# Kernel optimization log

Measured on AMD Instinct MI355X. Metric: run time of the kernel, lower is better.

Reference implementation:

```python
import jax, jax.numpy as jnp
import numpy as np

N = 1024      # num_nodes
U = 64        # num_units
IN_DIM = 2    # input feature dim per node
B = 32        # batch
F = IN_DIM + U  # 66, input_size inside _gconv


def _xavier(k, shape):
    fan_in, fan_out = shape[-2], shape[-1]
    std = (2.0 / (fan_in + fan_out)) ** 0.5
    return jax.random.normal(k, shape, jnp.float32) * std


def setup_inputs() -> dict:
    key = jax.random.key(0)
    ks = jax.random.split(key, 14)
    return {
        "inputs": jax.random.normal(ks[0], (B, N * IN_DIM), jnp.float32),
        "hx": jax.random.normal(ks[1], (B, N * U), jnp.float32),
        "adj": jax.random.uniform(ks[2], (2, N, N), jnp.float32),
        "mask": jax.random.uniform(ks[3], (8, N, N), jnp.float32),
        # gate gconv params (output_size = 2U). Note: torch LayerParams caches by
        # shape, so weights_s/weights_i/weights_bp are ONE shared weight, ditto atts/atti.
        "W_ru": _xavier(ks[4], (F, 2 * U)),
        "Watt_ru": _xavier(ks[5], (N, 2 * U, 2 * U)),
        "Watt1_ru": _xavier(ks[6], (N, 2 * U, 1)),
        "Wout_ru": _xavier(ks[7], (6 * U, 2 * U)),
        "b_ru": jnp.ones((2 * U,), jnp.float32),   # bias_start=1.0
        # candidate gconv params (output_size = U)
        "W_c": _xavier(ks[8], (F, U)),
        "Watt_c": _xavier(ks[9], (N, U, U)),
        "Watt1_c": _xavier(ks[10], (N, U, 1)),
        "Wout_c": _xavier(ks[11], (3 * U, U)),
        "b_c": jnp.zeros((U,), jnp.float32),
    }


def _gconv(inputs, state, adj, mask, W, Watt, Watt1, Wout, b):
    Bs = inputs.shape[0]
    x = jnp.concatenate([inputs.reshape(Bs, N, -1), state.reshape(Bs, N, -1)], axis=2)  # [B,N,F]
    Ff = x.shape[2]
    x0 = x.transpose(1, 2, 0).reshape(N, Ff * Bs)  # [N, F*B]
    a0, a1 = adj[0], adj[1]
    # supports in the exact order of the torch loop:
    # adj0, mask0..3*adj0, mask4..7*adj1, adj1  -> 10 matrices
    mats = jnp.concatenate(
        [a0[None], mask[:4] * a0[None], mask[4:] * a1[None], a1[None]], axis=0
    )  # [10,N,N]
    xk = jnp.einsum('mij,jf->mif', mats, x0)  # [10,N,F*B]
    x_all = jnp.concatenate([x0[None], xk], axis=0).reshape(11, N, Ff, Bs)
    x_bp = x_all[0].transpose(2, 0, 1)        # [B,N,F]
    x_i = x_all[1:6].transpose(3, 1, 0, 2)    # [B,N,5,F]
    x_s = x_all[6:].transpose(3, 1, 0, 2)     # [B,N,5,F]
    x_i_p = x_i @ W        # [B,N,5,O] (shared weight, see LayerParams shape cache)
    x_s_p = x_s @ W        # [B,N,5,O]
    x_bp_p = x_bp @ W      # [B,N,O]

    def attend(xp):
        h = jax.nn.relu(jnp.einsum('bnko,noq->bnkq', xp, Watt))     # per-node weights
        s = jnp.einsum('bnkq,nqo->bnko', h, Watt1)[..., 0]          # [B,N,5]
        a = jax.nn.softmax(s, axis=-1)                              # over 5 supports
        return jnp.einsum('bnk,bnko->bno', a, xp)                   # [B,N,O]

    xi = attend(x_i_p)
    xs = attend(x_s_p)
    out = jnp.concatenate([xi, xs, x_bp_p], axis=-1) @ Wout + b     # [B,N,O]
    return out.reshape(Bs, -1)


def reference(inputs, hx, adj, mask, W_ru, Watt_ru, Watt1_ru, Wout_ru, b_ru,
              W_c, Watt_c, Watt1_c, Wout_c, b_c):
    value = jax.nn.sigmoid(_gconv(inputs, hx, adj, mask, W_ru, Watt_ru, Watt1_ru, Wout_ru, b_ru))
    value = value.reshape(-1, N, 2 * U)
    r = value[..., :U].reshape(-1, N * U)
    u = value[..., U:].reshape(-1, N * U)
    c = jnp.tanh(_gconv(inputs, r * hx, adj, mask, W_c, Watt_c, Watt1_c, Wout_c, b_c))
    return u * hx + (1.0 - u) * c
```

## Files before the change

kernel.cpp:

```cpp
#include <hip/hip_runtime.h>
#include <hip/hip_fp16.h>
#include <cstdint>
#include <cstddef>

#define NN 1024
#define BB 32

typedef _Float16 f16x8 __attribute__((ext_vector_type(8)));
typedef _Float16 f16x4 __attribute__((ext_vector_type(4)));
typedef float f32x4 __attribute__((ext_vector_type(4)));

__device__ __forceinline__ void load_lds16(const void* g, void* l) {
  __builtin_amdgcn_global_load_lds(
      (const __attribute__((address_space(1))) void*)g,
      (__attribute__((address_space(3))) void*)l, 16, 0, 0);
}

__global__ __launch_bounds__(256) void k_build_amats(
    const float* __restrict__ adj, const float* __restrict__ mask,
    _Float16* __restrict__ A) {
  int q = blockIdx.x * 256 + threadIdx.x;
  int i = q >> 8;
  int j0 = (q & 255) << 2;
  size_t off = (size_t)i * 1024 + j0;
  float4 a0 = *(const float4*)(adj + off);
  float4 a1 = *(const float4*)(adj + (1u << 20) + off);
  f16x4 r;
  r[0] = a0.x; r[1] = a0.y; r[2] = a0.z; r[3] = a0.w;
  *(f16x4*)(A + off) = r;
  r[0] = a1.x; r[1] = a1.y; r[2] = a1.z; r[3] = a1.w;
  *(f16x4*)(A + (size_t)9 * 1048576 + off) = r;
#pragma unroll
  for (int l = 0; l < 8; ++l) {
    float4 mk = *(const float4*)(mask + (size_t)l * 1048576 + off);
    float4 base = (l < 4) ? a0 : a1;
    r[0] = mk.x * base.x; r[1] = mk.y * base.y;
    r[2] = mk.z * base.z; r[3] = mk.w * base.w;
    *(f16x4*)(A + (size_t)(l + 1) * 1048576 + off) = r;
  }
}

__global__ __launch_bounds__(256) void k_prep_wout(
    const float* __restrict__ Wru, const float* __restrict__ Wc,
    _Float16* __restrict__ WThru, _Float16* __restrict__ WTlru,
    _Float16* __restrict__ WThc, _Float16* __restrict__ WTlc) {
  int id = blockIdx.x * 256 + threadIdx.x;
  if (id < 128 * 384) {
    int o = id & 127, k = id >> 7;
    float w = Wru[k * 128 + o];
    _Float16 h = (_Float16)w;
    WThru[o * 384 + k] = h;
    WTlru[o * 384 + k] = (_Float16)(w - (float)h);
  } else {
    int id2 = id - 128 * 384;
    if (id2 < 64 * 192) {
      int o = id2 & 63, k = id2 >> 6;
      float w = Wc[k * 64 + o];
      _Float16 h = (_Float16)w;
      WThc[o * 192 + k] = h;
      WTlc[o * 192 + k] = (_Float16)(w - (float)h);
    }
  }
}

__global__ __launch_bounds__(256) void k_build_x0p(
    const float* __restrict__ inp, const float* __restrict__ state,
    _Float16* __restrict__ X0P) {
  const int b = blockIdx.x;
  const int j0 = blockIdx.y * 64;
  const int tid = threadIdx.x;
  for (int p = tid; p < 4096; p += 256) {
    int jj = p >> 6, f = p & 63;
    X0P[((size_t)(b * 1024 + j0 + jj)) * 96 + 2 + f] =
        (_Float16)state[(size_t)b * 65536 + (j0 + jj) * 64 + f];
  }
  if (tid < 128) {
    int jj = tid >> 1, f = tid & 1;
    X0P[((size_t)(b * 1024 + j0 + jj)) * 96 + f] =
        (_Float16)inp[(size_t)b * 2048 + (j0 + jj) * 2 + f];
    X0P[((size_t)(b * 1024 + j0 + 32 + jj)) * 96 + f] =
        (_Float16)inp[(size_t)b * 2048 + (j0 + 32 + jj) * 2 + f];
  }
  for (int p = tid; p < 64 * 32; p += 256) {
    int jj = p >> 5, f = 66 + (p & 31);
    if (f < 96)
      X0P[((size_t)(b * 1024 + j0 + jj)) * 96 + f] = (_Float16)0.f;
  }
}

template <int O>
__global__ __launch_bounds__(256, 2) void k_proj0_mfma(
    const _Float16* __restrict__ X0P, const float* __restrict__ W,
    _Float16* __restrict__ XP0, _Float16* __restrict__ XP0T) {
  constexpr int WR = O / 64;
  constexpr int WC = 4 / WR;
  constexpr int TN = WC * 64;
  constexpr int NPT = TN / 64;
  __shared__ _Float16 ldsB[2][TN * 32];
  const int tid = threadIdx.x;
  const int c0 = blockIdx.x * TN;
  const int b = c0 >> 10;
  const int l = tid & 63;
  const int w = tid >> 6;
  const int wr = w / WC, wc = w % WC;

  f16x8 af[4][3];
#pragma unroll
  for (int i = 0; i < 4; ++i) {
    int o = wr * 64 + i * 16 + (l & 15);
#pragma unroll
    for (int ks = 0; ks < 3; ++ks) {
#pragma unroll
      for (int e = 0; e < 8; ++e) {
        int f = ks * 32 + (l >> 4) * 8 + e;
        af[i][ks][e] = (f < 66) ? (_Float16)W[f * O + o] : (_Float16)0.f;
      }
    }
  }

  int tt[NPT], rr[NPT], qq[NPT];
#pragma unroll
  for (int u = 0; u < NPT; ++u) {
    tt[u] = u * 256 + tid;
    rr[u] = tt[u] >> 2;
    qq[u] = (tt[u] & 3) ^ (rr[u] & 3);
  }

  const int ps = ((l >> 4) ^ (l & 3)) * 8;
  int offB[4];
#pragma unroll
  for (int j = 0; j < 4; ++j)
    offB[j] = (wc * 64 + j * 16 + (l & 15)) * 32 + ps;

  f32x4 acc[4][4];
#pragma unroll
  for (int i = 0; i < 4; ++i)
#pragma unroll
    for (int j = 0; j < 4; ++j) acc[i][j] = (f32x4){0.f, 0.f, 0.f, 0.f};

#pragma unroll
  for (int u = 0; u < NPT; ++u)
    load_lds16(X0P + (size_t)(c0 + rr[u]) * 96 + qq[u] * 8,
               &ldsB[0][0] + tt[u] * 8);

  int buf = 0;
  for (int kt = 0; kt < 3; ++kt) {
    __syncthreads();
    if (kt + 1 < 3) {
#pragma unroll
      for (int u = 0; u < NPT; ++u)
        load_lds16(X0P + (size_t)(c0 + rr[u]) * 96 + (kt + 1) * 32 + qq[u] * 8,
                   &ldsB[buf ^ 1][0] + tt[u] * 8);
    }
    f16x8 bf[4];
#pragma unroll
    for (int j = 0; j < 4; ++j) bf[j] = *(const f16x8*)(&ldsB[buf][offB[j]]);
#pragma unroll
    for (int i = 0; i < 4; ++i)
#pragma unroll
      for (int j = 0; j < 4; ++j)
        acc[i][j] = __builtin_amdgcn_mfma_f32_16x16x32_f16(af[i][kt], bf[j],
                                                           acc[i][j], 0, 0, 0);
    buf ^= 1;
  }

#pragma unroll
  for (int i = 0; i < 4; ++i) {
    int ob = wr * 64 + i * 16 + (l >> 4) * 4;
#pragma unroll
    for (int j = 0; j < 4; ++j) {
      int jn = (c0 & 1023) + wc * 64 + j * 16 + (l & 15);
      f16x4 hv;
#pragma unroll
      for (int r = 0; r < 4; ++r) {
        hv[r] = (_Float16)acc[i][j][r];
        XP0T[((size_t)b * O + ob + r) * 1024 + jn] = hv[r];
      }
      *(f16x4*)(XP0 + ((size_t)jn * 32 + b) * O + ob) = hv;
    }
  }
}

template <int CN>
__global__ __launch_bounds__(256, 4) void k_supports2_mfma(
    const _Float16* __restrict__ A, const _Float16* __restrict__ BT,
    _Float16* __restrict__ XPD) {
  __shared__ _Float16 ldsA[2][4096];
  __shared__ _Float16 ldsB[2][4096];
  const int tid = threadIdx.x;
  const int bn = blockIdx.x;
  const int bm = blockIdx.y;
  const int l = tid & 63;
  const int w = tid >> 6;
  const int wr = w >> 1, wc = w & 1;

  const int t0 = tid, t1 = 256 + tid;
  const int r0 = t0 >> 2, q0 = (t0 & 3) ^ (r0 & 3);
  const int r1 = t1 >> 2, q1 = (t1 & 3) ^ (r1 & 3);
  const _Float16* gA0 = A + ((size_t)(bm * 128 + r0)) * 1024 + q0 * 8;
  const _Float16* gA1 = A + ((size_t)(bm * 128 + r1)) * 1024 + q1 * 8;
  const _Float16* gB0 = BT + ((size_t)(bn * 128 + r0)) * 1024 + q0 * 8;
  const _Float16* gB1 = BT + ((size_t)(bn * 128 + r1)) * 1024 + q1 * 8;

  const int ps = ((l >> 4) ^ (l & 3)) * 8;
  int offA[4], offB[4];
#pragma unroll
  for (int i = 0; i < 4; ++i) {
    offA[i] = (wr * 64 + i * 16 + (l & 15)) * 32 + ps;
    offB[i] = (wc * 64 + i * 16 + (l & 15)) * 32 + ps;
  }

  f32x4 acc[4][4];
#pragma unroll
  for (int i = 0; i < 4; ++i)
#pragma unroll
    for (int j = 0; j < 4; ++j) acc[i][j] = (f32x4){0.f, 0.f, 0.f, 0.f};

  load_lds16(gA0, &ldsA[0][0] + t0 * 8);
  load_lds16(gA1, &ldsA[0][0] + t1 * 8);
  load_lds16(gB0, &ldsB[0][0] + t0 * 8);
  load_lds16(gB1, &ldsB[0][0] + t1 * 8);

  int buf = 0;
  for (int kt = 0; kt < 32; ++kt) {
    __syncthreads();
    if (kt + 1 < 32) {
      int k0 = (kt + 1) * 32;
      load_lds16(gA0 + k0, &ldsA[buf ^ 1][0] + t0 * 8);
      load_lds16(gA1 + k0, &ldsA[buf ^ 1][0] + t1 * 8);
      load_lds16(gB0 + k0, &ldsB[buf ^ 1][0] + t0 * 8);
      load_lds16(gB1 + k0, &ldsB[buf ^ 1][0] + t1 * 8);
    }
    f16x8 af[4], bf[4];
#pragma unroll
    for (int i = 0; i < 4; ++i)
      af[i] = *(const f16x8*)(&ldsA[buf][offA[i]]);
#pragma unroll
    for (int i = 0; i < 4; ++i)
      bf[i] = *(const f16x8*)(&ldsB[buf][offB[i]]);
#pragma unroll
    for (int i = 0; i < 4; ++i)
#pragma unroll
      for (int j = 0; j < 4; ++j)
        acc[i][j] = __builtin_amdgcn_mfma_f32_16x16x32_f16(af[i], bf[j],
                                                           acc[i][j], 0, 0, 0);
    buf ^= 1;
  }

#pragma unroll
  for (int i = 0; i < 4; ++i) {
    int R = bm * 128 + wr * 64 + i * 16 + (l >> 4) * 4;
#pragma unroll
    for (int j = 0; j < 4; ++j) {
      int col = bn * 128 + wc * 64 + j * 16 + (l & 15);
#pragma unroll
      for (int r = 0; r < 4; ++r)
        XPD[(size_t)(R + r) * CN + col] = (_Float16)acc[i][j][r];
    }
  }
}

template <int O>
__global__ __launch_bounds__(256) void k_attend_mfma(
    const __half* __restrict__ XPD, const float* __restrict__ Watt,
    const float* __restrict__ Watt1, _Float16* __restrict__ CAT2h,
    _Float16* __restrict__ CAT2l) {
  constexpr int MTW = O / 64;
  constexpr int KS = O / 32;
  constexpr int SLOTS = O / 8;
  constexpr int SWZ = SLOTS - 1;
  const int n = blockIdx.x;
  const int tid = threadIdx.x;
  const int l = tid & 63;
  const int w = tid >> 6;

  __shared__ _Float16 xpL[160 * O];
  __shared__ float sPartL[4][160];
  __shared__ float aL[32][5];

  const int qbase = w * (O / 4);
  f16x8 afr[MTW][KS];
#pragma unroll
  for (int mt = 0; mt < MTW; ++mt) {
    const int q = qbase + mt * 16 + (l & 15);
#pragma unroll
    for (int ks = 0; ks < KS; ++ks) {
#pragma unroll
      for (int e = 0; e < 8; ++e) {
        int o = ks * 32 + (l >> 4) * 8 + e;
        afr[mt][ks][e] = (_Float16)Watt[((size_t)n * O + o) * O + q];
      }
    }
  }
  float wt1[MTW][4];
#pragma unroll
  for (int mt = 0; mt < MTW; ++mt)
#pragma unroll
    for (int r = 0; r < 4; ++r)
      wt1[mt][r] = Watt1[(size_t)n * O + qbase + mt * 16 + (l >> 4) * 4 + r];

  for (int g = 0; g < 2; ++g) {
    if (g) __syncthreads();
    {
      const f16x8* xsrc = reinterpret_cast<const f16x8*>(XPD);
      f16x8* xdst = reinterpret_cast<f16x8*>(xpL);
      for (int p = tid; p < 160 * SLOTS; p += 256) {
        int row = p / SLOTS;
        int sc = p - row * SLOTS;
        int phys = sc ^ (row & SWZ);
        int si = row >> 5, b = row & 31;
        size_t gi = ((size_t)(g * 5 + si) * 1024 + n) * (size_t)(4 * O) +
                    b * (O / 8) + sc;
        xdst[row * SLOTS + phys] = xsrc[gi];
      }
    }
    __syncthreads();

    for (int nt = 0; nt < 10; ++nt) {
      f32x4 acc[MTW];
#pragma unroll
      for (int mt = 0; mt < MTW; ++mt) acc[mt] = (f32x4){0.f, 0.f, 0.f, 0.f};
      const int row = nt * 16 + (l & 15);
#pragma unroll
      for (int ks = 0; ks < KS; ++ks) {
        int phys = (ks * 4 + (l >> 4)) ^ (row & SWZ);
        f16x8 bf = *(const f16x8*)(&xpL[row * O + phys * 8]);
#pragma unroll
        for (int mt = 0; mt < MTW; ++mt)
          acc[mt] = __builtin_amdgcn_mfma_f32_16x16x32_f16(afr[mt][ks], bf,
                                                           acc[mt], 0, 0, 0);
      }
      float sp = 0.f;
#pragma unroll
      for (int mt = 0; mt < MTW; ++mt)
#pragma unroll
        for (int r = 0; r < 4; ++r)
          sp += fmaxf(acc[mt][r], 0.f) * wt1[mt][r];
      sp += __shfl_xor(sp, 16);
      sp += __shfl_xor(sp, 32);
      if (l < 16) sPartL[w][nt * 16 + l] = sp;
    }
    __syncthreads();

    if (tid < 32) {
      const int b = tid;
      float sv[5];
#pragma unroll
      for (int k = 0; k < 5; ++k) {
        int row = k * 32 + b;
        sv[k] = sPartL[0][row] + sPartL[1][row] + sPartL[2][row] +
                sPartL[3][row];
      }
      float mx = sv[0];
#pragma unroll
      for (int k = 1; k < 5; ++k) mx = fmaxf(mx, sv[k]);
      float e[5], sum = 0.f;
#pragma unroll
      for (int k = 0; k < 5; ++k) {
        e[k] = expf(sv[k] - mx);
        sum += e[k];
      }
      float inv = 1.f / sum;
#pragma unroll
      for (int k = 0; k < 5; ++k) aL[b][k] = e[k] * inv;
    }
    __syncthreads();

    for (int it = 0; it < SLOTS * 32 / 256; ++it) {
      int idx = it * 256 + tid;
      int b = idx & 31;
      int sc = idx >> 5;
      float o8[8] = {0.f, 0.f, 0.f, 0.f, 0.f, 0.f, 0.f, 0.f};
#pragma unroll
      for (int si = 0; si < 5; ++si) {
        int row = si * 32 + b;
        int phys = sc ^ (row & SWZ);
        f16x8 xv = *(const f16x8*)(&xpL[row * O + phys * 8]);
        float a = aL[b][si];
#pragma unroll
        for (int j = 0; j < 8; ++j) o8[j] += a * (float)xv[j];
      }
      f16x8 hv, lv;
#pragma unroll
      for (int j = 0; j < 8; ++j) {
        hv[j] = (_Float16)o8[j];
        lv[j] = (_Float16)(o8[j] - (float)hv[j]);
      }
      size_t doff = ((size_t)n * 32 + b) * (2 * O) + g * O + sc * 8;
      *reinterpret_cast<f16x8*>(CAT2h + doff) = hv;
      *reinterpret_cast<f16x8*>(CAT2l + doff) = lv;
    }
  }
}

__global__ __launch_bounds__(256, 2) void k_wout_ru_mfma(
    const _Float16* __restrict__ CAT2h, const _Float16* __restrict__ CAT2l,
    const _Float16* __restrict__ XP0, const _Float16* __restrict__ WTh,
    const _Float16* __restrict__ WTl, const float* __restrict__ bias,
    const float* __restrict__ hx, float* __restrict__ RHX,
    float* __restrict__ UBUF) {
  constexpr int KTOT = 384, KC = 8, KT = 12;
  __shared__ _Float16 ldsAh[2][4096];
  __shared__ _Float16 ldsAl[2][4096];
  __shared__ _Float16 ldsBh[2][4096];
  __shared__ _Float16 ldsBl[2][4096];
  const int tid = threadIdx.x;
  const int blk = blockIdx.x;
  const int l = tid & 63;
  const int w = tid >> 6;
  const int wr = w >> 1, wc = w & 1;

  const int t0 = tid, t1 = 256 + tid;
  const int r0 = t0 >> 2, q0 = (t0 & 3) ^ (r0 & 3);
  const int r1 = t1 >> 2, q1 = (t1 & 3) ^ (r1 & 3);
  const size_t R0 = (size_t)blk * 128 + r0, R1 = (size_t)blk * 128 + r1;
  const _Float16* pA0ch = CAT2h + R0 * 256 + q0 * 8;
  const _Float16* pA1ch = CAT2h + R1 * 256 + q1 * 8;
  const _Float16* pA0cl = CAT2l + R0 * 256 + q0 * 8;
  const _Float16* pA1cl = CAT2l + R1 * 256 + q1 * 8;
  const _Float16* pA0x = XP0 + R0 * 128 + q0 * 8;
  const _Float16* pA1x = XP0 + R1 * 128 + q1 * 8;
  const _Float16* pB0h = WTh + (size_t)r0 * KTOT + q0 * 8;
  const _Float16* pB1h = WTh + (size_t)r1 * KTOT + q1 * 8;
  const _Float16* pB0l = WTl + (size_t)r0 * KTOT + q0 * 8;
  const _Float16* pB1l = WTl + (size_t)r1 * KTOT + q1 * 8;

  const int ps = ((l >> 4) ^ (l & 3)) * 8;
  int offA[4], offB[4];
#pragma unroll
  for (int i = 0; i < 4; ++i) {
    offA[i] = (wr * 64 + i * 16 + (l & 15)) * 32 + ps;
    offB[i] = (wc * 64 + i * 16 + (l & 15)) * 32 + ps;
  }

  f32x4 acc[4][4];
#pragma unroll
  for (int i = 0; i < 4; ++i)
#pragma unroll
    for (int j = 0; j < 4; ++j) acc[i][j] = (f32x4){0.f, 0.f, 0.f, 0.f};

  load_lds16(pA0ch, &ldsAh[0][0] + t0 * 8);
  load_lds16(pA1ch, &ldsAh[0][0] + t1 * 8);
  load_lds16(pA0cl, &ldsAl[0][0] + t0 * 8);
  load_lds16(pA1cl, &ldsAl[0][0] + t1 * 8);
  load_lds16(pB0h, &ldsBh[0][0] + t0 * 8);
  load_lds16(pB1h, &ldsBh[0][0] + t1 * 8);
  load_lds16(pB0l, &ldsBl[0][0] + t0 * 8);
  load_lds16(pB1l, &ldsBl[0][0] + t1 * 8);

  int buf = 0;
  for (int kt = 0; kt < KT; ++kt) {
    __syncthreads();
    if (kt + 1 < KT) {
      int k1 = kt + 1;
      const _Float16* a0 =
          (k1 < KC) ? pA0ch + k1 * 32 : pA0x + (k1 - KC) * 32;
      const _Float16* a1 =
          (k1 < KC) ? pA1ch + k1 * 32 : pA1x + (k1 - KC) * 32;
      load_lds16(a0, &ldsAh[buf ^ 1][0] + t0 * 8);
      load_lds16(a1, &ldsAh[buf ^ 1][0] + t1 * 8);
      if (k1 < KC) {
        load_lds16(pA0cl + k1 * 32, &ldsAl[buf ^ 1][0] + t0 * 8);
        load_lds16(pA1cl + k1 * 32, &ldsAl[buf ^ 1][0] + t1 * 8);
      }
      load_lds16(pB0h + k1 * 32, &ldsBh[buf ^ 1][0] + t0 * 8);
      load_lds16(pB1h + k1 * 32, &ldsBh[buf ^ 1][0] + t1 * 8);
      load_lds16(pB0l + k1 * 32, &ldsBl[buf ^ 1][0] + t0 * 8);
      load_lds16(pB1l + k1 * 32, &ldsBl[buf ^ 1][0] + t1 * 8);
    }
    f16x8 ah[4], bh[4], bl[4];
#pragma unroll
    for (int i = 0; i < 4; ++i) ah[i] = *(const f16x8*)(&ldsAh[buf][offA[i]]);
#pragma unroll
    for (int i = 0; i < 4; ++i) bh[i] = *(const f16x8*)(&ldsBh[buf][offB[i]]);
#pragma unroll
    for (int i = 0; i < 4; ++i) bl[i] = *(const f16x8*)(&ldsBl[buf][offB[i]]);
#pragma unroll
    for (int i = 0; i < 4; ++i)
#pragma unroll
      for (int j = 0; j < 4; ++j) {
        acc[i][j] = __builtin_amdgcn_mfma_f32_16x16x32_f16(ah[i], bh[j],
                                                           acc[i][j], 0, 0, 0);
        acc[i][j] = __builtin_amdgcn_mfma_f32_16x16x32_f16(ah[i], bl[j],
                                                           acc[i][j], 0, 0, 0);
      }
    if (kt < KC) {
      f16x8 al[4];
#pragma unroll
      for (int i = 0; i < 4; ++i)
        al[i] = *(const f16x8*)(&ldsAl[buf][offA[i]]);
#pragma unroll
      for (int i = 0; i < 4; ++i)
#pragma unroll
        for (int j = 0; j < 4; ++j)
          acc[i][j] = __builtin_amdgcn_mfma_f32_16x16x32_f16(al[i], bh[j],
                                                             acc[i][j], 0, 0, 0);
    }
    buf ^= 1;
  }

#pragma unroll
  for (int i = 0; i < 4; ++i) {
    int R = blk * 128 + wr * 64 + i * 16 + (l >> 4) * 4;
#pragma unroll
    for (int j = 0; j < 4; ++j) {
      int o = wc * 64 + j * 16 + (l & 15);
      float bv = bias[o];
#pragma unroll
      for (int rr = 0; rr < 4; ++rr) {
        int Rr = R + rr;
        int n = Rr >> 5, b = Rr & 31;
        size_t base = ((size_t)b * NN + n) * 64;
        float val = 1.f / (1.f + expf(-(acc[i][j][rr] + bv)));
        if (o < 64)
          RHX[base + o] = val * hx[base + o];
        else
          UBUF[base + (o - 64)] = val;
      }
    }
  }
}

__global__ __launch_bounds__(256, 2) void k_wout_c_mfma(
    const _Float16* __restrict__ CAT2h, const _Float16* __restrict__ XP0,
    const _Float16* __restrict__ WTh, const float* __restrict__ bias,
    const float* __restrict__ UBUF, const float* __restrict__ hx,
    float* __restrict__ out) {
  constexpr int KTOT = 192, KC = 4, KT = 6;
  __shared__ _Float16 ldsAh[2][4096];
  __shared__ _Float16 ldsBh[2][2048];
  const int tid = threadIdx.x;
  const int blk = blockIdx.x;
  const int l = tid & 63;
  const int w = tid >> 6;

  const int t0 = tid, t1 = 256 + tid;
  const int r0 = t0 >> 2, q0 = (t0 & 3) ^ (r0 & 3);
  const int r1 = t1 >> 2, q1 = (t1 & 3) ^ (r1 & 3);
  const size_t R0 = (size_t)blk * 128 + r0, R1 = (size_t)blk * 128 + r1;
  const _Float16* pA0ch = CAT2h + R0 * 128 + q0 * 8;
  const _Float16* pA1ch = CAT2h + R1 * 128 + q1 * 8;
  const _Float16* pA0x = XP0 + R0 * 64 + q0 * 8;
  const _Float16* pA1x = XP0 + R1 * 64 + q1 * 8;
  const int rb = tid >> 2, qb = (tid & 3) ^ (rb & 3);
  const _Float16* pBh = WTh + (size_t)rb * KTOT + qb * 8;

  const int ps = ((l >> 4) ^ (l & 3)) * 8;
  int offA[2], offB[4];
#pragma unroll
  for (int i = 0; i < 2; ++i)
    offA[i] = (w * 32 + i * 16 + (l & 15)) * 32 + ps;
#pragma unroll
  for (int j = 0; j < 4; ++j) offB[j] = (j * 16 + (l & 15)) * 32 + ps;

  f32x4 acc[2][4];
#pragma unroll
  for (int i = 0; i < 2; ++i)
#pragma unroll
    for (int j = 0; j < 4; ++j) acc[i][j] = (f32x4){0.f, 0.f, 0.f, 0.f};

  load_lds16(pA0ch, &ldsAh[0][0] + t0 * 8);
  load_lds16(pA1ch, &ldsAh[0][0] + t1 * 8);
  load_lds16(pBh, &ldsBh[0][0] + tid * 8);

  int buf = 0;
  for (int kt = 0; kt < KT; ++kt) {
    __syncthreads();
    if (kt + 1 < KT) {
      int k1 = kt + 1;
      const _Float16* a0 =
          (k1 < KC) ? pA0ch + k1 * 32 : pA0x + (k1 - KC) * 32;
      const _Float16* a1 =
          (k1 < KC) ? pA1ch + k1 * 32 : pA1x + (k1 - KC) * 32;
      load_lds16(a0, &ldsAh[buf ^ 1][0] + t0 * 8);
      load_lds16(a1, &ldsAh[buf ^ 1][0] + t1 * 8);
      load_lds16(pBh + k1 * 32, &ldsBh[buf ^ 1][0] + tid * 8);
    }
    f16x8 ah[2], bh[4];
#pragma unroll
    for (int i = 0; i < 2; ++i) ah[i] = *(const f16x8*)(&ldsAh[buf][offA[i]]);
#pragma unroll
    for (int j = 0; j < 4; ++j) bh[j] = *(const f16x8*)(&ldsBh[buf][offB[j]]);
#pragma unroll
    for (int i = 0; i < 2; ++i)
#pragma unroll
      for (int j = 0; j < 4; ++j)
        acc[i][j] = __builtin_amdgcn_mfma_f32_16x16x32_f16(ah[i], bh[j],
                                                           acc[i][j], 0, 0, 0);
    buf ^= 1;
  }

#pragma unroll
  for (int i = 0; i < 2; ++i) {
    int R = blk * 128 + w * 32 + i * 16 + (l >> 4) * 4;
#pragma unroll
    for (int j = 0; j < 4; ++j) {
      int o = j * 16 + (l & 15);
      float bv = bias[o];
#pragma unroll
      for (int rr = 0; rr < 4; ++rr) {
        int Rr = R + rr;
        int n = Rr >> 5, b = Rr & 31;
        size_t idx = ((size_t)b * NN + n) * 64 + o;
        float cval = tanhf(acc[i][j][rr] + bv);
        float u = UBUF[idx];
        out[idx] = u * hx[idx] + (1.f - u) * cval;
      }
    }
  }
}

extern "C" void kernel_launch(void* const* d_in, const int* in_sizes, int n_in,
                              void* d_out, int out_size, void* d_ws,
                              size_t ws_size, hipStream_t stream) {
  const float* inputs   = (const float*)d_in[0];
  const float* hx       = (const float*)d_in[1];
  const float* adj      = (const float*)d_in[2];
  const float* mask     = (const float*)d_in[3];
  const float* W_ru     = (const float*)d_in[4];
  const float* Watt_ru  = (const float*)d_in[5];
  const float* Watt1_ru = (const float*)d_in[6];
  const float* Wout_ru  = (const float*)d_in[7];
  const float* b_ru     = (const float*)d_in[8];
  const float* W_c      = (const float*)d_in[9];
  const float* Watt_c   = (const float*)d_in[10];
  const float* Watt1_c  = (const float*)d_in[11];
  const float* Wout_c   = (const float*)d_in[12];
  const float* b_c      = (const float*)d_in[13];

  char* ws = (char*)d_ws;
  _Float16*  X0P   = (_Float16*)(ws);
  _Float16*  XPD   = (_Float16*)(ws + 6291456);
  _Float16*  XP0   = (_Float16*)(ws + 90177536);
  _Float16*  XP0T  = (_Float16*)(ws + 98566144);
  _Float16*  CAT2h = (_Float16*)(ws + 106954752);
  _Float16*  CAT2l = (_Float16*)(ws + 123731968);
  float*     RHX   = (float*)(ws + 140509184);
  float*     UBUF  = (float*)(ws + 148897792);
  _Float16*  A_all = (_Float16*)(ws + 157286400);
  _Float16*  WThru = (_Float16*)(ws + 178257920);
  _Float16*  WTlru = (_Float16*)(ws + 178356224);
  _Float16*  WThc  = (_Float16*)(ws + 178454528);
  _Float16*  WTlc  = (_Float16*)(ws + 178479104);
  float*     out   = (float*)d_out;

  k_build_amats<<<1024, 256, 0, stream>>>(adj, mask, A_all);
  k_prep_wout<<<240, 256, 0, stream>>>(Wout_ru, Wout_c, WThru, WTlru, WThc,
                                       WTlc);

  k_build_x0p<<<dim3(32, 16), 256, 0, stream>>>(inputs, hx, X0P);
  k_proj0_mfma<128><<<256, 256, 0, stream>>>(X0P, W_ru, XP0, XP0T);
  k_supports2_mfma<4096><<<dim3(32, 80), 256, 0, stream>>>(A_all, XP0T, XPD);
  k_attend_mfma<128><<<1024, 256, 0, stream>>>((const __half*)XPD, Watt_ru,
                                               Watt1_ru, CAT2h, CAT2l);
  k_wout_ru_mfma<<<256, 256, 0, stream>>>(CAT2h, CAT2l, XP0, WThru, WTlru,
                                          b_ru, hx, RHX, UBUF);
  k_build_x0p<<<dim3(32, 16), 256, 0, stream>>>(inputs, RHX, X0P);
  k_proj0_mfma<64><<<128, 256, 0, stream>>>(X0P, W_c, XP0, XP0T);
  k_supports2_mfma<2048><<<dim3(16, 80), 256, 0, stream>>>(A_all, XP0T, XPD);
  k_attend_mfma<64><<<1024, 256, 0, stream>>>((const __half*)XPD, Watt_c,
                                              Watt1_c, CAT2h, CAT2l);
  k_wout_c_mfma<<<256, 256, 0, stream>>>(CAT2h, XP0, WThc, b_c,
                                         UBUF, hx, out);
}
```

Measured before the change: 340.0 us.

## Fuse x0 packing into projection, merge prep kernels, stage GEMM epilogue via LDS

Merges the adjacency/mask build and the Wout transpose into one prep launch. Folds the fp32-to-fp16 packing of inputs and state directly into the projection kernel, so the X0P buffer and its two build launches go away. The supports GEMM now writes its output tile through a swizzled LDS staging buffer and emits coalesced 16-byte stores instead of scattered 2-byte stores, with launch bounds lowered to 2 blocks per CU. This cuts launches and global round trips, at the cost of possibly lower occupancy in the supports kernel.

```diff
diff --git a/kernel.cpp b/kernel.cpp
--- a/kernel.cpp
+++ b/kernel.cpp
@@ -16,87 +16,65 @@
       (__attribute__((address_space(3))) void*)l, 16, 0, 0);
 }
 
-__global__ __launch_bounds__(256) void k_build_amats(
+__global__ __launch_bounds__(256) void k_prep(
     const float* __restrict__ adj, const float* __restrict__ mask,
-    _Float16* __restrict__ A) {
-  int q = blockIdx.x * 256 + threadIdx.x;
-  int i = q >> 8;
-  int j0 = (q & 255) << 2;
-  size_t off = (size_t)i * 1024 + j0;
-  float4 a0 = *(const float4*)(adj + off);
-  float4 a1 = *(const float4*)(adj + (1u << 20) + off);
-  f16x4 r;
-  r[0] = a0.x; r[1] = a0.y; r[2] = a0.z; r[3] = a0.w;
-  *(f16x4*)(A + off) = r;
-  r[0] = a1.x; r[1] = a1.y; r[2] = a1.z; r[3] = a1.w;
-  *(f16x4*)(A + (size_t)9 * 1048576 + off) = r;
-#pragma unroll
-  for (int l = 0; l < 8; ++l) {
-    float4 mk = *(const float4*)(mask + (size_t)l * 1048576 + off);
-    float4 base = (l < 4) ? a0 : a1;
-    r[0] = mk.x * base.x; r[1] = mk.y * base.y;
-    r[2] = mk.z * base.z; r[3] = mk.w * base.w;
-    *(f16x4*)(A + (size_t)(l + 1) * 1048576 + off) = r;
-  }
-}
-
-__global__ __launch_bounds__(256) void k_prep_wout(
-    const float* __restrict__ Wru, const float* __restrict__ Wc,
-    _Float16* __restrict__ WThru, _Float16* __restrict__ WTlru,
-    _Float16* __restrict__ WThc, _Float16* __restrict__ WTlc) {
-  int id = blockIdx.x * 256 + threadIdx.x;
-  if (id < 128 * 384) {
-    int o = id & 127, k = id >> 7;
-    float w = Wru[k * 128 + o];
-    _Float16 h = (_Float16)w;
-    WThru[o * 384 + k] = h;
-    WTlru[o * 384 + k] = (_Float16)(w - (float)h);
+    _Float16* __restrict__ A, const float* __restrict__ Wru,
+    const float* __restrict__ Wc, _Float16* __restrict__ WThru,
+    _Float16* __restrict__ WTlru, _Float16* __restrict__ WThc,
+    _Float16* __restrict__ WTlc) {
+  const int bid = blockIdx.x;
+  const int tid = threadIdx.x;
+  if (bid < 1024) {
+    int q = bid * 256 + tid;
+    int i = q >> 8;
+    int j0 = (q & 255) << 2;
+    size_t off = (size_t)i * 1024 + j0;
+    float4 a0 = *(const float4*)(adj + off);
+    float4 a1 = *(const float4*)(adj + (1u << 20) + off);
+    f16x4 r;
+    r[0] = a0.x; r[1] = a0.y; r[2] = a0.z; r[3] = a0.w;
+    *(f16x4*)(A + off) = r;
+    r[0] = a1.x; r[1] = a1.y; r[2] = a1.z; r[3] = a1.w;
+    *(f16x4*)(A + (size_t)9 * 1048576 + off) = r;
+#pragma unroll
+    for (int l = 0; l < 8; ++l) {
+      float4 mk = *(const float4*)(mask + (size_t)l * 1048576 + off);
+      float4 base = (l < 4) ? a0 : a1;
+      r[0] = mk.x * base.x; r[1] = mk.y * base.y;
+      r[2] = mk.z * base.z; r[3] = mk.w * base.w;
+      *(f16x4*)(A + (size_t)(l + 1) * 1048576 + off) = r;
+    }
   } else {
-    int id2 = id - 128 * 384;
-    if (id2 < 64 * 192) {
-      int o = id2 & 63, k = id2 >> 6;
-      float w = Wc[k * 64 + o];
+    int id = (bid - 1024) * 256 + tid;
+    if (id < 128 * 384) {
+      int o = id & 127, k = id >> 7;
+      float w = Wru[k * 128 + o];
       _Float16 h = (_Float16)w;
-      WThc[o * 192 + k] = h;
-      WTlc[o * 192 + k] = (_Float16)(w - (float)h);
-    }
-  }
-}
-
-__global__ __launch_bounds__(256) void k_build_x0p(
+      WThru[o * 384 + k] = h;
+      WTlru[o * 384 + k] = (_Float16)(w - (float)h);
+    } else {
+      int id2 = id - 128 * 384;
+      if (id2 < 64 * 192) {
+        int o = id2 & 63, k = id2 >> 6;
+        float w = Wc[k * 64 + o];
+        _Float16 h = (_Float16)w;
+        WThc[o * 192 + k] = h;
+        WTlc[o * 192 + k] = (_Float16)(w - (float)h);
+      }
+    }
+  }
+}
+
+template <int O>
+__global__ __launch_bounds__(256, 2) void k_proj0_fused(
     const float* __restrict__ inp, const float* __restrict__ state,
-    _Float16* __restrict__ X0P) {
-  const int b = blockIdx.x;
-  const int j0 = blockIdx.y * 64;
-  const int tid = threadIdx.x;
-  for (int p = tid; p < 4096; p += 256) {
-    int jj = p >> 6, f = p & 63;
-    X0P[((size_t)(b * 1024 + j0 + jj)) * 96 + 2 + f] =
-        (_Float16)state[(size_t)b * 65536 + (j0 + jj) * 64 + f];
-  }
-  if (tid < 128) {
-    int jj = tid >> 1, f = tid & 1;
-    X0P[((size_t)(b * 1024 + j0 + jj)) * 96 + f] =
-        (_Float16)inp[(size_t)b * 2048 + (j0 + jj) * 2 + f];
-    X0P[((size_t)(b * 1024 + j0 + 32 + jj)) * 96 + f] =
-        (_Float16)inp[(size_t)b * 2048 + (j0 + 32 + jj) * 2 + f];
-  }
-  for (int p = tid; p < 64 * 32; p += 256) {
-    int jj = p >> 5, f = 66 + (p & 31);
-    if (f < 96)
-      X0P[((size_t)(b * 1024 + j0 + jj)) * 96 + f] = (_Float16)0.f;
-  }
-}
-
-template <int O>
-__global__ __launch_bounds__(256, 2) void k_proj0_mfma(
-    const _Float16* __restrict__ X0P, const float* __restrict__ W,
-    _Float16* __restrict__ XP0, _Float16* __restrict__ XP0T) {
+    const float* __restrict__ W, _Float16* __restrict__ XP0,
+    _Float16* __restrict__ XP0T) {
   constexpr int WR = O / 64;
   constexpr int WC = 4 / WR;
   constexpr int TN = WC * 64;
-  constexpr int NPT = TN / 64;
-  __shared__ _Float16 ldsB[2][TN * 32];
+  constexpr int TPR = 256 / TN;
+  __shared__ _Float16 ldsX[TN * 96];
   const int tid = threadIdx.x;
   const int c0 = blockIdx.x * TN;
   const int b = c0 >> 10;
@@ -118,19 +96,64 @@
     }
   }
 
-  int tt[NPT], rr[NPT], qq[NPT];
-#pragma unroll
-  for (int u = 0; u < NPT; ++u) {
-    tt[u] = u * 256 + tid;
-    rr[u] = tt[u] >> 2;
-    qq[u] = (tt[u] & 3) ^ (rr[u] & 3);
-  }
+  {
+    const int row = (TPR == 2) ? (tid >> 1) : tid;
+    const int h = (TPR == 2) ? (tid & 1) : 0;
+    const int j = (c0 & 1023) + row;
+    const float* sp = state + (size_t)b * 65536 + (size_t)j * 64;
+    _Float16* ldsRow = ldsX + row * 96;
+    const int rsw = row & 3;
+    if (TPR == 1 || h == 0) {
+      float2 in2 = *(const float2*)(inp + (size_t)b * 2048 + j * 2);
+      float sv[48];
+#pragma unroll
+      for (int u = 0; u < 12; ++u)
+        *(f32x4*)(sv + u * 4) = *(const f32x4*)(sp + u * 4);
+      f16x8 v;
+      v[0] = (_Float16)in2.x;
+      v[1] = (_Float16)in2.y;
+#pragma unroll
+      for (int e = 2; e < 8; ++e) v[e] = (_Float16)sv[e - 2];
+      *(f16x8*)(ldsRow + ((0 ^ rsw) << 3)) = v;
+#pragma unroll
+      for (int c = 1; c < 6; ++c) {
+#pragma unroll
+        for (int e = 0; e < 8; ++e) v[e] = (_Float16)sv[c * 8 + e - 2];
+        int kt = c >> 2, cq = c & 3;
+        *(f16x8*)(ldsRow + kt * 32 + ((cq ^ rsw) << 3)) = v;
+      }
+    }
+    if (TPR == 1 || h == 1) {
+      float sv2[20];
+#pragma unroll
+      for (int u = 0; u < 5; ++u)
+        *(f32x4*)(sv2 + u * 4) = *(const f32x4*)(sp + 44 + u * 4);
+      f16x8 v;
+#pragma unroll
+      for (int e = 0; e < 8; ++e) v[e] = (_Float16)sv2[2 + e];
+      *(f16x8*)(ldsRow + 32 + ((2 ^ rsw) << 3)) = v;
+#pragma unroll
+      for (int e = 0; e < 8; ++e) v[e] = (_Float16)sv2[10 + e];
+      *(f16x8*)(ldsRow + 32 + ((3 ^ rsw) << 3)) = v;
+      v[0] = (_Float16)sv2[18];
+      v[1] = (_Float16)sv2[19];
+#pragma unroll
+      for (int e = 2; e < 8; ++e) v[e] = (_Float16)0.f;
+      *(f16x8*)(ldsRow + 64 + ((0 ^ rsw) << 3)) = v;
+#pragma unroll
+      for (int e = 0; e < 8; ++e) v[e] = (_Float16)0.f;
+      *(f16x8*)(ldsRow + 64 + ((1 ^ rsw) << 3)) = v;
+      *(f16x8*)(ldsRow + 64 + ((2 ^ rsw) << 3)) = v;
+      *(f16x8*)(ldsRow + 64 + ((3 ^ rsw) << 3)) = v;
+    }
+  }
+  __syncthreads();
 
   const int ps = ((l >> 4) ^ (l & 3)) * 8;
   int offB[4];
 #pragma unroll
   for (int j = 0; j < 4; ++j)
-    offB[j] = (wc * 64 + j * 16 + (l & 15)) * 32 + ps;
+    offB[j] = (wc * 64 + j * 16 + (l & 15)) * 96 + ps;
 
   f32x4 acc[4][4];
 #pragma unroll
@@ -139,29 +162,17 @@
     for (int j = 0; j < 4; ++j) acc[i][j] = (f32x4){0.f, 0.f, 0.f, 0.f};
 
 #pragma unroll
-  for (int u = 0; u < NPT; ++u)
-    load_lds16(X0P + (size_t)(c0 + rr[u]) * 96 + qq[u] * 8,
-               &ldsB[0][0] + tt[u] * 8);
-
-  int buf = 0;
   for (int kt = 0; kt < 3; ++kt) {
-    __syncthreads();
-    if (kt + 1 < 3) {
-#pragma unroll
-      for (int u = 0; u < NPT; ++u)
-        load_lds16(X0P + (size_t)(c0 + rr[u]) * 96 + (kt + 1) * 32 + qq[u] * 8,
-                   &ldsB[buf ^ 1][0] + tt[u] * 8);
-    }
     f16x8 bf[4];
 #pragma unroll
-    for (int j = 0; j < 4; ++j) bf[j] = *(const f16x8*)(&ldsB[buf][offB[j]]);
+    for (int j = 0; j < 4; ++j)
+      bf[j] = *(const f16x8*)(&ldsX[offB[j] + kt * 32]);
 #pragma unroll
     for (int i = 0; i < 4; ++i)
 #pragma unroll
       for (int j = 0; j < 4; ++j)
         acc[i][j] = __builtin_amdgcn_mfma_f32_16x16x32_f16(af[i][kt], bf[j],
                                                            acc[i][j], 0, 0, 0);
-    buf ^= 1;
   }
 
 #pragma unroll
@@ -182,11 +193,10 @@
 }
 
 template <int CN>
-__global__ __launch_bounds__(256, 4) void k_supports2_mfma(
+__global__ __launch_bounds__(256, 2) void k_supports2_mfma(
     const _Float16* __restrict__ A, const _Float16* __restrict__ BT,
     _Float16* __restrict__ XPD) {
-  __shared__ _Float16 ldsA[2][4096];
-  __shared__ _Float16 ldsB[2][4096];
+  __shared__ _Float16 ldsU[4][4096];
   const int tid = threadIdx.x;
   const int bn = blockIdx.x;
   const int bm = blockIdx.y;
@@ -216,28 +226,28 @@
 #pragma unroll
     for (int j = 0; j < 4; ++j) acc[i][j] = (f32x4){0.f, 0.f, 0.f, 0.f};
 
-  load_lds16(gA0, &ldsA[0][0] + t0 * 8);
-  load_lds16(gA1, &ldsA[0][0] + t1 * 8);
-  load_lds16(gB0, &ldsB[0][0] + t0 * 8);
-  load_lds16(gB1, &ldsB[0][0] + t1 * 8);
+  load_lds16(gA0, &ldsU[0][0] + t0 * 8);
+  load_lds16(gA1, &ldsU[0][0] + t1 * 8);
+  load_lds16(gB0, &ldsU[2][0] + t0 * 8);
+  load_lds16(gB1, &ldsU[2][0] + t1 * 8);
 
   int buf = 0;
   for (int kt = 0; kt < 32; ++kt) {
     __syncthreads();
     if (kt + 1 < 32) {
       int k0 = (kt + 1) * 32;
-      load_lds16(gA0 + k0, &ldsA[buf ^ 1][0] + t0 * 8);
-      load_lds16(gA1 + k0, &ldsA[buf ^ 1][0] + t1 * 8);
-      load_lds16(gB0 + k0, &ldsB[buf ^ 1][0] + t0 * 8);
-      load_lds16(gB1 + k0, &ldsB[buf ^ 1][0] + t1 * 8);
+      load_lds16(gA0 + k0, &ldsU[buf ^ 1][0] + t0 * 8);
+      load_lds16(gA1 + k0, &ldsU[buf ^ 1][0] + t1 * 8);
+      load_lds16(gB0 + k0, &ldsU[2 + (buf ^ 1)][0] + t0 * 8);
+      load_lds16(gB1 + k0, &ldsU[2 + (buf ^ 1)][0] + t1 * 8);
     }
     f16x8 af[4], bf[4];
 #pragma unroll
     for (int i = 0; i < 4; ++i)
-      af[i] = *(const f16x8*)(&ldsA[buf][offA[i]]);
+      af[i] = *(const f16x8*)(&ldsU[buf][offA[i]]);
 #pragma unroll
     for (int i = 0; i < 4; ++i)
-      bf[i] = *(const f16x8*)(&ldsB[buf][offB[i]]);
+      bf[i] = *(const f16x8*)(&ldsU[2 + buf][offB[i]]);
 #pragma unroll
     for (int i = 0; i < 4; ++i)
 #pragma unroll
@@ -247,15 +257,31 @@
     buf ^= 1;
   }
 
-#pragma unroll
-  for (int i = 0; i < 4; ++i) {
-    int R = bm * 128 + wr * 64 + i * 16 + (l >> 4) * 4;
-#pragma unroll
-    for (int j = 0; j < 4; ++j) {
-      int col = bn * 128 + wc * 64 + j * 16 + (l & 15);
-#pragma unroll
-      for (int r = 0; r < 4; ++r)
-        XPD[(size_t)(R + r) * CN + col] = (_Float16)acc[i][j][r];
+  __syncthreads();
+  {
+    _Float16* C = &ldsU[0][0];
+#pragma unroll
+    for (int i = 0; i < 4; ++i) {
+      int Rl = wr * 64 + i * 16 + (l >> 4) * 4;
+#pragma unroll
+      for (int j = 0; j < 4; ++j) {
+        int Cc = wc * 64 + j * 16 + (l & 15);
+#pragma unroll
+        for (int r = 0; r < 4; ++r) {
+          int row = Rl + r;
+          C[row * 128 + (((Cc >> 3) ^ (row & 7)) << 3) + (Cc & 7)] =
+              (_Float16)acc[i][j][r];
+        }
+      }
+    }
+    __syncthreads();
+#pragma unroll
+    for (int it = 0; it < 8; ++it) {
+      int flat = it * 256 + tid;
+      int row = flat >> 4;
+      int c2 = flat & 15;
+      f16x8 v = *(const f16x8*)(&C[row * 128 + ((c2 ^ (row & 7)) << 3)]);
+      *(f16x8*)(XPD + (size_t)(bm * 128 + row) * CN + bn * 128 + c2 * 8) = v;
     }
   }
 }
@@ -629,7 +655,6 @@
   const float* b_c      = (const float*)d_in[13];
 
   char* ws = (char*)d_ws;
-  _Float16*  X0P   = (_Float16*)(ws);
   _Float16*  XPD   = (_Float16*)(ws + 6291456);
   _Float16*  XP0   = (_Float16*)(ws + 90177536);
   _Float16*  XP0T  = (_Float16*)(ws + 98566144);
@@ -644,19 +669,16 @@
   _Float16*  WTlc  = (_Float16*)(ws + 178479104);
   float*     out   = (float*)d_out;
 
-  k_build_amats<<<1024, 256, 0, stream>>>(adj, mask, A_all);
-  k_prep_wout<<<240, 256, 0, stream>>>(Wout_ru, Wout_c, WThru, WTlru, WThc,
-                                       WTlc);
-
-  k_build_x0p<<<dim3(32, 16), 256, 0, stream>>>(inputs, hx, X0P);
-  k_proj0_mfma<128><<<256, 256, 0, stream>>>(X0P, W_ru, XP0, XP0T);
+  k_prep<<<1264, 256, 0, stream>>>(adj, mask, A_all, Wout_ru, Wout_c, WThru,
+                                   WTlru, WThc, WTlc);
+
+  k_proj0_fused<128><<<256, 256, 0, stream>>>(inputs, hx, W_ru, XP0, XP0T);
   k_supports2_mfma<4096><<<dim3(32, 80), 256, 0, stream>>>(A_all, XP0T, XPD);
   k_attend_mfma<128><<<1024, 256, 0, stream>>>((const __half*)XPD, Watt_ru,
                                                Watt1_ru, CAT2h, CAT2l);
   k_wout_ru_mfma<<<256, 256, 0, stream>>>(CAT2h, CAT2l, XP0, WThru, WTlru,
                                           b_ru, hx, RHX, UBUF);
-  k_build_x0p<<<dim3(32, 16), 256, 0, stream>>>(inputs, RHX, X0P);
-  k_proj0_mfma<64><<<128, 256, 0, stream>>>(X0P, W_c, XP0, XP0T);
+  k_proj0_fused<64><<<128, 256, 0, stream>>>(inputs, RHX, W_c, XP0, XP0T);
   k_supports2_mfma<2048><<<dim3(16, 80), 256, 0, stream>>>(A_all, XP0T, XPD);
   k_attend_mfma<64><<<1024, 256, 0, stream>>>((const __half*)XPD, Watt_c,
                                               Watt1_c, CAT2h, CAT2l);
```

Measured after the change: 316.4 us. 1.07x faster.
